# Kernel tuning notes

Hardware: AMD Instinct MI355X
Metric: run time of the kernel (lower is better)

Reference implementation:

```python
import jax, jax.numpy as jnp
import numpy as np

B, NSIDE, NH = 4, 64, 8
N = 12 * NSIDE * NSIDE          # HEALPix pixel count, nested ordering
CIN, CHID, COUT = 256, 512, 256
WS = 16                          # window = 4**(w+1) nested pixels, w=1
HD = CHID // NH


def _ln(x, g, b, eps=1e-5):
    m = x.mean(-1, keepdims=True)
    v = ((x - m) ** 2).mean(-1, keepdims=True)
    return (x - m) * jax.lax.rsqrt(v + eps) * g + b


def _win_attn(x, qkv_w, qkv_b, pw, pb):
    b_, n_, c = x.shape
    nw = n_ // WS
    xw = x.reshape(b_, nw, WS, c)
    qkv = xw @ qkv_w + qkv_b                      # [B, nw, ws, 3C]
    q, k, v = jnp.split(qkv, 3, axis=-1)
    def heads(t):
        return t.reshape(b_, nw, WS, NH, HD).transpose(0, 1, 3, 2, 4)
    q, k, v = heads(q), heads(k), heads(v)        # [B, nw, H, ws, hd]
    a = jax.nn.softmax(jnp.einsum('bwhqd,bwhkd->bwhqk', q, k) * (HD ** -0.5), axis=-1)
    o = jnp.einsum('bwhqk,bwhkd->bwhqd', a, v)
    o = o.transpose(0, 1, 3, 2, 4).reshape(b_, n_, c)
    return o @ pw + pb


def _heal_block(x, p, shift):
    if shift:
        x = jnp.roll(x, -WS // 2, axis=1)          # shifted-window (cyclic in nested order)
    x = x + _win_attn(_ln(x, p['ln1g'], p['ln1b']), p['qkvw'], p['qkvb'], p['pw'], p['pb'])
    h = _ln(x, p['ln2g'], p['ln2b'])
    h = jax.nn.gelu(h @ p['m1w'] + p['m1b'], approximate=False) @ p['m2w'] + p['m2b']
    x = x + h
    if shift:
        x = jnp.roll(x, WS // 2, axis=1)
    return x


def _sn_linear(h, W, b, u):
    # torch spectral_norm: one power-iteration, u/v detached, sigma = u' W v
    v = W @ u                                      # [CHID]
    v = jax.lax.stop_gradient(v / (jnp.linalg.norm(v) + 1e-12))
    u2 = v @ W                                     # [COUT]
    u2 = jax.lax.stop_gradient(u2 / (jnp.linalg.norm(u2) + 1e-12))
    sigma = v @ W @ u2
    return h @ (W / sigma) + b


def setup_inputs() -> dict:
    key = jax.random.key(0)
    ks = iter(jax.random.split(key, 64))
    def w(shape, s=0.02):
        return jax.random.normal(next(ks), shape, jnp.float32) * s
    inp = {'x': jax.random.normal(next(ks), (B, N, CIN), jnp.float32)}
    inp['ff1_w'] = w((CIN, CHID)); inp['ff1_b'] = jnp.zeros((CHID,), jnp.float32)
    for pre in ('a', 'b'):
        inp[f'{pre}_ln1g'] = jnp.ones((CHID,), jnp.float32)
        inp[f'{pre}_ln1b'] = jnp.zeros((CHID,), jnp.float32)
        inp[f'{pre}_qkvw'] = w((CHID, 3 * CHID)); inp[f'{pre}_qkvb'] = jnp.zeros((3 * CHID,), jnp.float32)
        inp[f'{pre}_pw'] = w((CHID, CHID)); inp[f'{pre}_pb'] = jnp.zeros((CHID,), jnp.float32)
        inp[f'{pre}_ln2g'] = jnp.ones((CHID,), jnp.float32)
        inp[f'{pre}_ln2b'] = jnp.zeros((CHID,), jnp.float32)
        inp[f'{pre}_m1w'] = w((CHID, 4 * CHID)); inp[f'{pre}_m1b'] = jnp.zeros((4 * CHID,), jnp.float32)
        inp[f'{pre}_m2w'] = w((4 * CHID, CHID)); inp[f'{pre}_m2b'] = jnp.zeros((CHID,), jnp.float32)
    inp['ff2_w'] = w((CHID, COUT)); inp['ff2_b'] = jnp.zeros((COUT,), jnp.float32)
    inp['ff2_u'] = jax.random.normal(next(ks), (COUT,), jnp.float32)
    return inp


def reference(x, ff1_w, ff1_b,
              a_ln1g, a_ln1b, a_qkvw, a_qkvb, a_pw, a_pb, a_ln2g, a_ln2b, a_m1w, a_m1b, a_m2w, a_m2b,
              b_ln1g, b_ln1b, b_qkvw, b_qkvb, b_pw, b_pb, b_ln2g, b_ln2b, b_m1w, b_m1b, b_m2w, b_m2b,
              ff2_w, ff2_b, ff2_u):
    pa = dict(ln1g=a_ln1g, ln1b=a_ln1b, qkvw=a_qkvw, qkvb=a_qkvb, pw=a_pw, pb=a_pb,
              ln2g=a_ln2g, ln2b=a_ln2b, m1w=a_m1w, m1b=a_m1b, m2w=a_m2w, m2b=a_m2b)
    pb_ = dict(ln1g=b_ln1g, ln1b=b_ln1b, qkvw=b_qkvw, qkvb=b_qkvb, pw=b_pw, pb=b_pb,
               ln2g=b_ln2g, ln2b=b_ln2b, m1w=b_m1w, m1b=b_m1b, m2w=b_m2w, m2b=b_m2b)
    h = jax.nn.gelu(x @ ff1_w + ff1_b, approximate=False)   # feed_forward1
    h = _heal_block(h, pa, shift=False)                     # message_passing1
    h = _heal_block(h, pb_, shift=True)                     # message_passing2
    return _sn_linear(h, ff2_w, ff2_b, ff2_u)               # spectral-norm linear
```

## Files before the change

### kernel.cpp

```cpp
#include <hip/hip_runtime.h>
#include <hip/hip_bf16.h>
#include <math.h>

typedef _Float16 f16;
typedef __attribute__((ext_vector_type(8))) _Float16 f16x8;
typedef __attribute__((ext_vector_type(4))) float f32x4;

#define DINLINE __device__ __forceinline__

DINLINE float gelu_exact(float x) {
  return 0.5f * x * (1.0f + erff(x * 0.70710678118654752f));
}
DINLINE void gload16(const void* g, void* l) {
  __builtin_amdgcn_global_load_lds((const __attribute__((address_space(1))) void*)g,
                                   (__attribute__((address_space(3))) void*)l, 16, 0, 0);
}

#define BAR       __builtin_amdgcn_s_barrier()
#define WAITLGKM  asm volatile("s_waitcnt lgkmcnt(0)" ::: "memory")
#define WAITVM(n) asm volatile("s_waitcnt vmcnt(" #n ")" ::: "memory")

template <int EPI>
__global__ __launch_bounds__(512, 2) void gemm256(
    const f16* __restrict__ A, const f16* __restrict__ Bt,
    const float* __restrict__ bias, const f16* __restrict__ Cin,
    float* __restrict__ Cf, f16* __restrict__ Cb,
    const float* __restrict__ scale_ptr,
    int N, int K, int nct)
{
  __shared__ alignas(16) f16 sm[2][4][8192];

  const int nwg = (int)gridDim.x;
  const int gid = (int)blockIdx.x;
  const int q = nwg >> 3, r = nwg & 7;
  const int xcd = gid & 7, idx = gid >> 3;
  const int swz = (xcd < r ? xcd * (q + 1) : r * (q + 1) + (xcd - r) * q) + idx;
  const int rt = swz / nct, ct = swz - rt * nct;
  const int m0 = rt << 8, n0 = ct << 8;

  const int tid = (int)threadIdx.x;
  const int lane = tid & 63;
  const int wid = tid >> 6;
  const int wr = wid >> 2, wc = wid & 3;

  const int srow = tid >> 2;
  const int sl = (tid & 3) ^ ((srow >> 1) & 3);
  const size_t aG = (size_t)(m0 + srow) * K + sl * 8;
  const size_t bG = (size_t)(n0 + srow) * K + sl * 8;
  const int sL = tid * 8;

  const int rsel = lane & 15, khi = lane >> 4;
  const int sx = (khi ^ ((rsel >> 1) & 3)) << 3;

  f32x4 acc[8][4] = {};
  f16x8 aF[4], bF[4];

  const int NT = K >> 6;

#define STAGEH(h)                                                             \
  {                                                                           \
    const int _t = (h) >> 2, _r = (h) & 3, _b = _t & 1;                       \
    const f16* _s = (_r & 1) ? Bt : A;                                        \
    const size_t _g = ((_r & 1) ? bG : aG) + (size_t)_t * 64 + ((_r >> 1) << 5); \
    gload16(_s + _g, &sm[_b][_r][sL]);                                        \
    gload16(_s + _g + (size_t)128 * (size_t)K, &sm[_b][_r][4096 + sL]);       \
  }

#define DSRA(b, kc, mb)                                                       \
  {                                                                           \
    _Pragma("unroll")                                                         \
    for (int _i = 0; _i < 4; ++_i)                                            \
      aF[_i] = *(const f16x8*)(&sm[b][(kc) << 1]                              \
                  [(wr * 128 + ((mb) + _i) * 16 + rsel) * 32 + sx]);          \
  }

#define DSRB(b, kc)                                                           \
  {                                                                           \
    _Pragma("unroll")                                                         \
    for (int _i = 0; _i < 4; ++_i)                                            \
      bF[_i] = *(const f16x8*)(&sm[b][1 + ((kc) << 1)]                        \
                  [(wc * 64 + _i * 16 + rsel) * 32 + sx]);                    \
  }

#define MMC(mb)                                                               \
  {                                                                           \
    __builtin_amdgcn_s_setprio(1);                                            \
    _Pragma("unroll")                                                         \
    for (int _m = 0; _m < 4; ++_m)                                            \
      _Pragma("unroll")                                                       \
      for (int _n = 0; _n < 4; ++_n)                                          \
        acc[(mb) + _m][_n] = __builtin_amdgcn_mfma_f32_16x16x32_f16(          \
            aF[_m], bF[_n], acc[(mb) + _m][_n], 0, 0, 0);                     \
    __builtin_amdgcn_s_setprio(0);                                            \
  }

  STAGEH(0); STAGEH(1); STAGEH(2); STAGEH(3); STAGEH(4);
  WAITVM(6);
  BAR;

  for (int t = 0; t < NT - 2; ++t) {
    const int b = t & 1, hb = 4 * t;
    STAGEH(hb + 5); DSRA(b, 0, 0); DSRB(b, 0); BAR; WAITLGKM; MMC(0); WAITVM(6); BAR;
    STAGEH(hb + 6); DSRA(b, 0, 4);             BAR; WAITLGKM; MMC(4); WAITVM(6); BAR;
    STAGEH(hb + 7); DSRA(b, 1, 0); DSRB(b, 1); BAR; WAITLGKM; MMC(0); WAITVM(6); BAR;
    STAGEH(hb + 8); DSRA(b, 1, 4);             BAR; WAITLGKM; MMC(4); WAITVM(6); BAR;
  }
  {
    const int t = NT - 2, b = t & 1, hb = 4 * t;
    STAGEH(hb + 5); DSRA(b, 0, 0); DSRB(b, 0); BAR; WAITLGKM; MMC(0); WAITVM(6); BAR;
    STAGEH(hb + 6); DSRA(b, 0, 4);             BAR; WAITLGKM; MMC(4); WAITVM(6); BAR;
    STAGEH(hb + 7); DSRA(b, 1, 0); DSRB(b, 1); BAR; WAITLGKM; MMC(0); WAITVM(6); BAR;
                    DSRA(b, 1, 4);             BAR; WAITLGKM; MMC(4); WAITVM(4); BAR;
  }
  {
    const int b = (NT - 1) & 1;
    DSRA(b, 0, 0); DSRB(b, 0); BAR; WAITLGKM; MMC(0); WAITVM(2); BAR;
    DSRA(b, 0, 4);             BAR; WAITLGKM; MMC(4); WAITVM(0); BAR;
    DSRA(b, 1, 0); DSRB(b, 1); BAR; WAITLGKM; MMC(0); BAR;
    DSRA(b, 1, 4);             BAR; WAITLGKM; MMC(4); BAR;
  }

  const float scale = (EPI & 8) ? scale_ptr[0] : 1.0f;
  const int R0 = m0 + wr * 128, C0 = n0 + wc * 64;
  f16* myr = (f16*)&sm[0][0][0] + wid * 8192;
#pragma unroll
  for (int m = 0; m < 8; ++m) {
#pragma unroll
    for (int n = 0; n < 4; ++n) {
      const int col = C0 + n * 16 + rsel;
      const float bb = bias ? bias[col] : 0.0f;
#pragma unroll
      for (int j = 0; j < 4; ++j) {
        const int rl = m * 16 + khi * 4 + j;
        const int row = R0 + rl;
        float v = acc[m][n][j] * scale + bb;
        if (EPI & 1) v = gelu_exact(v);
        if (EPI & 2) v += (float)Cin[(size_t)row * N + col];
        if (EPI & 4) myr[rl * 64 + n * 16 + rsel] = (f16)v;
        else         Cf[(size_t)row * N + col] = v;
      }
    }
  }
  if (EPI & 4) {
    asm volatile("" ::: "memory");
#pragma unroll
    for (int ci = 0; ci < 16; ++ci) {
      const int rl = ci * 8 + (lane >> 3);
      f16x8 v8 = *(const f16x8*)(myr + rl * 64 + (lane & 7) * 8);
      *(f16x8*)(Cb + (size_t)(R0 + rl) * N + C0 + (lane & 7) * 8) = v8;
    }
  }
#undef STAGEH
#undef DSRA
#undef DSRB
#undef MMC
}

__global__ __launch_bounds__(256) void ln_f16(
    const f16* __restrict__ X, const float* __restrict__ g,
    const float* __restrict__ b, f16* __restrict__ Y)
{
  const int token = blockIdx.x * 4 + (threadIdx.x >> 6);
  const int lane = threadIdx.x & 63;
  f16x8 v = *(const f16x8*)(X + (size_t)token * 512 + lane * 8);
  float vf[8];
  float s = 0.f, s2 = 0.f;
#pragma unroll
  for (int j = 0; j < 8; ++j) { vf[j] = (float)v[j]; s += vf[j]; s2 += vf[j] * vf[j]; }
#pragma unroll
  for (int o = 32; o > 0; o >>= 1) { s += __shfl_xor(s, o, 64); s2 += __shfl_xor(s2, o, 64); }
  const float mean = s * (1.f / 512.f);
  const float inv = rsqrtf(s2 * (1.f / 512.f) - mean * mean + 1e-5f);
  const int c = lane * 8;
  f32x4 g0 = *(const f32x4*)(g + c), g1 = *(const f32x4*)(g + c + 4);
  f32x4 b0 = *(const f32x4*)(b + c), b1 = *(const f32x4*)(b + c + 4);
  f16x8 o8;
#pragma unroll
  for (int j = 0; j < 4; ++j) {
    o8[j]     = (f16)((vf[j] - mean) * inv * g0[j] + b0[j]);
    o8[4 + j] = (f16)((vf[4 + j] - mean) * inv * g1[j] + b1[j]);
  }
  *(f16x8*)(Y + (size_t)token * 512 + c) = o8;
}

__global__ __launch_bounds__(256) void cvt_f32_f16(const float* __restrict__ X,
                                                   f16* __restrict__ Y, long n8)
{
  const long i = (long)blockIdx.x * 256 + threadIdx.x;
  if (i >= n8) return;
  f32x4 v0 = *(const f32x4*)(X + i * 8), v1 = *(const f32x4*)(X + i * 8 + 4);
  f16x8 o8;
#pragma unroll
  for (int j = 0; j < 4; ++j) { o8[j] = (f16)v0[j]; o8[4 + j] = (f16)v1[j]; }
  *(f16x8*)(Y + i * 8) = o8;
}

__global__ __launch_bounds__(256) void w_tr(const float* __restrict__ W,
                                            f16* __restrict__ Wt, int K, int N)
{
  const int t = blockIdx.x * 256 + threadIdx.x;
  if (t >= K * N) return;
  const int n = t / K, k = t - n * K;
  Wt[t] = (f16)W[(size_t)k * N + n];
}

template <int SHIFT>
__global__ __launch_bounds__(256) void win_attn(const f16* __restrict__ QKV,
                                                f16* __restrict__ O)
{
  __shared__ alignas(16) f16 kv[2][16][1160];
  const int wl0 = (int)blockIdx.x * 2;
  const int tid = (int)threadIdx.x;

  for (int i = tid; i < 4096; i += 256) {
    const int win = i >> 11;
    const int rem = i & 2047;
    const int row = rem >> 7;
    const int c8 = rem & 127;
    const int src = ((wl0 + win) * 16 + row + SHIFT) % 49152;
    const int sect = c8 >> 6;
    const int hh = (c8 >> 3) & 7;
    const int dd = (c8 & 7) * 8;
    *(f16x8*)(&kv[win][row][sect * 576 + hh * 72 + dd]) =
        *(const f16x8*)(QKV + (size_t)src * 1536 + 512 + c8 * 8);
  }

  const int win = tid >> 7, h = (tid >> 4) & 7, qi = tid & 15;
  const int qtok = ((wl0 + win) * 16 + qi + SHIFT) % 49152;
  f16x8 qv[8];
#pragma unroll
  for (int c8 = 0; c8 < 8; ++c8)
    qv[c8] = *(const f16x8*)(QKV + (size_t)qtok * 1536 + h * 64 + c8 * 8);

  __syncthreads();

  float sc[16];
  float mx = -1e30f;
#pragma unroll
  for (int kj = 0; kj < 16; ++kj) {
    const f16* kr = &kv[win][kj][h * 72];
    float s = 0.f;
#pragma unroll
    for (int c8 = 0; c8 < 8; ++c8) {
      f16x8 k8 = *(const f16x8*)(kr + c8 * 8);
#pragma unroll
      for (int j = 0; j < 8; ++j) s += (float)qv[c8][j] * (float)k8[j];
    }
    s *= 0.125f;
    sc[kj] = s;
    mx = fmaxf(mx, s);
  }
  float sum = 0.f;
#pragma unroll
  for (int kj = 0; kj < 16; ++kj) { sc[kj] = expf(sc[kj] - mx); sum += sc[kj]; }
  const float inv = 1.f / sum;
  float ov[64] = {};
#pragma unroll
  for (int kj = 0; kj < 16; ++kj) {
    const float a = sc[kj] * inv;
    const f16* vr = &kv[win][kj][576 + h * 72];
#pragma unroll
    for (int c8 = 0; c8 < 8; ++c8) {
      f16x8 v8 = *(const f16x8*)(vr + c8 * 8);
#pragma unroll
      for (int j = 0; j < 8; ++j) ov[c8 * 8 + j] += a * (float)v8[j];
    }
  }
  f16* orow = O + (size_t)qtok * 512 + h * 64;
#pragma unroll
  for (int c8 = 0; c8 < 8; ++c8) {
    f16x8 t;
#pragma unroll
    for (int j = 0; j < 8; ++j) t[j] = (f16)ov[c8 * 8 + j];
    *(f16x8*)(orow + c8 * 8) = t;
  }
}

__global__ __launch_bounds__(256) void sn_sigma(const float* __restrict__ W,
                                                const float* __restrict__ u,
                                                float* __restrict__ inv_sigma)
{
  __shared__ float vsh[512];
  __shared__ float ush[256];
  __shared__ float red[256];
  const int t = (int)threadIdx.x;
  ush[t] = u[t];
  __syncthreads();
  float a0 = 0.f, a1 = 0.f;
  for (int j = 0; j < 256; ++j) {
    a0 += W[t * 256 + j] * ush[j];
    a1 += W[(t + 256) * 256 + j] * ush[j];
  }
  vsh[t] = a0; vsh[t + 256] = a1;
  red[t] = a0 * a0 + a1 * a1;
  __syncthreads();
  for (int s = 128; s > 0; s >>= 1) { if (t < s) red[t] += red[t + s]; __syncthreads(); }
  const float nv = sqrtf(red[0]) + 1e-12f;
  __syncthreads();
  const float invv = 1.f / nv;
  vsh[t] *= invv; vsh[t + 256] *= invv;
  __syncthreads();
  float u2 = 0.f;
  for (int i = 0; i < 512; ++i) u2 += vsh[i] * W[i * 256 + t];
  red[t] = u2 * u2;
  __syncthreads();
  for (int s = 128; s > 0; s >>= 1) { if (t < s) red[t] += red[t + s]; __syncthreads(); }
  const float nu = sqrtf(red[0]) + 1e-12f;
  __syncthreads();
  ush[t] = u2 / nu;
  __syncthreads();
  float d0 = 0.f, d1 = 0.f;
  for (int j = 0; j < 256; ++j) {
    d0 += W[t * 256 + j] * ush[j];
    d1 += W[(t + 256) * 256 + j] * ush[j];
  }
  red[t] = vsh[t] * d0 + vsh[t + 256] * d1;
  __syncthreads();
  for (int s = 128; s > 0; s >>= 1) { if (t < s) red[t] += red[t + s]; __syncthreads(); }
  if (t == 0) inv_sigma[0] = 1.f / red[0];
}

__global__ void fill_sentinel(float* __restrict__ out, long n, float val)
{
  const long i = (long)blockIdx.x * 256 + threadIdx.x;
  for (long k = i; k < n; k += (long)gridDim.x * 256) out[k] = val;
}

extern "C" void kernel_launch(void* const* d_in, const int* in_sizes, int n_in,
                              void* d_out, int out_size, void* d_ws, size_t ws_size,
                              hipStream_t stream)
{
  const int M = 196608;
  const int MC = 49152;
  constexpr size_t OFF_U   = 201326592ull;
  constexpr size_t OFF_OH  = 201326592ull + 150994944ull;
  constexpr size_t OFF_WT  = 402653184ull;
  constexpr size_t OFF_SIG = 415760384ull;
  constexpr size_t NEED    = OFF_SIG + 256ull;

  if (ws_size < NEED) {
    fill_sentinel<<<2048, 256, 0, stream>>>((float*)d_out, (long)out_size,
                                            (float)(ws_size >> 20));
    return;
  }

  char* ws = (char*)d_ws;
  f16* R     = (f16*)(ws);
  f16* U     = (f16*)(ws + OFF_U);
  f16* OH    = (f16*)(ws + OFF_OH);
  f16* WT    = (f16*)(ws + OFF_WT);
  float* sig = (float*)(ws + OFF_SIG);
  f16* X     = (f16*)d_out;

  const float* ff1_b = (const float*)d_in[2];
  const float* ff2_b = (const float*)d_in[28];

  f16* W_FF1 = WT;
  auto W_QKV = [&](int blk) { return WT + (blk ? 3276800 : 131072); };
  auto W_PW  = [&](int blk) { return WT + (blk ? 4063232 : 917504); };
  auto W_M1  = [&](int blk) { return WT + (blk ? 4325376 : 1179648); };
  auto W_M2  = [&](int blk) { return WT + (blk ? 5373952 : 2228224); };
  f16* W_FF2 = WT + 6422528;

  w_tr<<<512, 256, 0, stream>>>((const float*)d_in[1], W_FF1, 256, 512);
  for (int blk = 0; blk < 2; ++blk) {
    w_tr<<<3072, 256, 0, stream>>>((const float*)d_in[blk ? 17 : 5], W_QKV(blk), 512, 1536);
    w_tr<<<1024, 256, 0, stream>>>((const float*)d_in[blk ? 19 : 7], W_PW(blk), 512, 512);
    w_tr<<<4096, 256, 0, stream>>>((const float*)d_in[blk ? 23 : 11], W_M1(blk), 512, 2048);
    w_tr<<<4096, 256, 0, stream>>>((const float*)d_in[blk ? 25 : 13], W_M2(blk), 2048, 512);
  }
  w_tr<<<512, 256, 0, stream>>>((const float*)d_in[27], W_FF2, 512, 256);
  sn_sigma<<<1, 256, 0, stream>>>((const float*)d_in[27], (const float*)d_in[29], sig);

  cvt_f32_f16<<<24576, 256, 0, stream>>>((const float*)d_in[0], U, (long)M * 256 / 8);
  gemm256<5><<<1536, 512, 0, stream>>>(U, W_FF1, ff1_b, nullptr, nullptr, R, nullptr,
                                       512, 256, 2);

  for (int blk = 0; blk < 2; ++blk) {
    const float* ln1g = (const float*)d_in[blk ? 15 : 3];
    const float* ln1b = (const float*)d_in[blk ? 16 : 4];
    const float* qkvb = (const float*)d_in[blk ? 18 : 6];
    const float* pb   = (const float*)d_in[blk ? 20 : 8];
    const float* ln2g = (const float*)d_in[blk ? 21 : 9];
    const float* ln2b = (const float*)d_in[blk ? 22 : 10];
    const float* m1b  = (const float*)d_in[blk ? 24 : 12];
    const float* m2b  = (const float*)d_in[blk ? 26 : 14];

    ln_f16<<<49152, 256, 0, stream>>>(R, ln1g, ln1b, X);
    for (int mc = 0; mc < 4; ++mc) {
      const size_t ro = (size_t)mc * MC * 512;
      gemm256<4><<<1152, 512, 0, stream>>>(X + ro, W_QKV(blk), qkvb, nullptr,
                                           nullptr, U, nullptr, 1536, 512, 6);
      if (blk == 0) win_attn<0><<<1536, 256, 0, stream>>>(U, OH);
      else          win_attn<8><<<1536, 256, 0, stream>>>(U, OH);
      gemm256<6><<<384, 512, 0, stream>>>(OH, W_PW(blk), pb, R + ro,
                                          nullptr, R + ro, nullptr, 512, 512, 2);
    }
    ln_f16<<<49152, 256, 0, stream>>>(R, ln2g, ln2b, X);
    for (int mc = 0; mc < 4; ++mc) {
      const size_t ro = (size_t)mc * MC * 512;
      gemm256<5><<<1536, 512, 0, stream>>>(X + ro, W_M1(blk), m1b, nullptr,
                                           nullptr, U, nullptr, 2048, 512, 8);
      gemm256<6><<<384, 512, 0, stream>>>(U, W_M2(blk), m2b, R + ro,
                                          nullptr, R + ro, nullptr, 512, 2048, 2);
    }
  }

  gemm256<8><<<768, 512, 0, stream>>>(R, W_FF2, ff2_b, nullptr, (float*)d_out,
                                      nullptr, sig, 256, 512, 1);
}
```

Baseline: 5.219 ms.

## Swap MFMA operands for direct vector epilogue, fast GELU, tiled weight transpose

Result: faster. 5.097 ms (-2.3%).

```diff
diff --git a/kernel.cpp b/kernel.cpp
--- a/kernel.cpp
+++ b/kernel.cpp
@@ -4,12 +4,15 @@
 
 typedef _Float16 f16;
 typedef __attribute__((ext_vector_type(8))) _Float16 f16x8;
+typedef __attribute__((ext_vector_type(4))) _Float16 f16x4;
 typedef __attribute__((ext_vector_type(4))) float f32x4;
 
 #define DINLINE __device__ __forceinline__
 
-DINLINE float gelu_exact(float x) {
-  return 0.5f * x * (1.0f + erff(x * 0.70710678118654752f));
+DINLINE float gelu_fast(float x) {
+  float t = 0.7978845608f * x * __builtin_fmaf(0.044715f * x, x, 1.0f);
+  float E = __expf(fminf(2.0f * t, 18.0f));
+  return x * E * __builtin_amdgcn_rcpf(E + 1.0f);
 }
 DINLINE void gload16(const void* g, void* l) {
   __builtin_amdgcn_global_load_lds((const __attribute__((address_space(1))) void*)g,
@@ -90,7 +93,7 @@
       _Pragma("unroll")                                                       \
       for (int _n = 0; _n < 4; ++_n)                                          \
         acc[(mb) + _m][_n] = __builtin_amdgcn_mfma_f32_16x16x32_f16(          \
-            aF[_m], bF[_n], acc[(mb) + _m][_n], 0, 0, 0);                     \
+            bF[_n], aF[_m], acc[(mb) + _m][_n], 0, 0, 0);                     \
     __builtin_amdgcn_s_setprio(0);                                            \
   }
 
@@ -122,32 +125,37 @@
 
   const float scale = (EPI & 8) ? scale_ptr[0] : 1.0f;
   const int R0 = m0 + wr * 128, C0 = n0 + wc * 64;
-  f16* myr = (f16*)&sm[0][0][0] + wid * 8192;
 #pragma unroll
   for (int m = 0; m < 8; ++m) {
+    const int row = R0 + m * 16 + rsel;
 #pragma unroll
     for (int n = 0; n < 4; ++n) {
-      const int col = C0 + n * 16 + rsel;
-      const float bb = bias ? bias[col] : 0.0f;
-#pragma unroll
-      for (int j = 0; j < 4; ++j) {
-        const int rl = m * 16 + khi * 4 + j;
-        const int row = R0 + rl;
-        float v = acc[m][n][j] * scale + bb;
-        if (EPI & 1) v = gelu_exact(v);
-        if (EPI & 2) v += (float)Cin[(size_t)row * N + col];
-        if (EPI & 4) myr[rl * 64 + n * 16 + rsel] = (f16)v;
-        else         Cf[(size_t)row * N + col] = v;
+      const int col = C0 + n * 16 + (khi << 2);
+      f32x4 v = acc[m][n];
+      if (EPI & 8) {
+#pragma unroll
+        for (int j = 0; j < 4; ++j) v[j] *= scale;
       }
-    }
-  }
-  if (EPI & 4) {
-    asm volatile("" ::: "memory");
-#pragma unroll
-    for (int ci = 0; ci < 16; ++ci) {
-      const int rl = ci * 8 + (lane >> 3);
-      f16x8 v8 = *(const f16x8*)(myr + rl * 64 + (lane & 7) * 8);
-      *(f16x8*)(Cb + (size_t)(R0 + rl) * N + C0 + (lane & 7) * 8) = v8;
+      f32x4 bb = *(const f32x4*)(bias + col);
+#pragma unroll
+      for (int j = 0; j < 4; ++j) v[j] += bb[j];
+      if (EPI & 1) {
+#pragma unroll
+        for (int j = 0; j < 4; ++j) v[j] = gelu_fast(v[j]);
+      }
+      if (EPI & 2) {
+        f16x4 c4 = *(const f16x4*)(Cin + (size_t)row * N + col);
+#pragma unroll
+        for (int j = 0; j < 4; ++j) v[j] += (float)c4[j];
+      }
+      if (EPI & 4) {
+        f16x4 o;
+#pragma unroll
+        for (int j = 0; j < 4; ++j) o[j] = (f16)v[j];
+        *(f16x4*)(Cb + (size_t)row * N + col) = o;
+      } else {
+        *(f32x4*)(Cf + (size_t)row * N + col) = v;
+      }
     }
   }
 #undef STAGEH
@@ -158,29 +166,31 @@
 
 __global__ __launch_bounds__(256) void ln_f16(
     const f16* __restrict__ X, const float* __restrict__ g,
-    const float* __restrict__ b, f16* __restrict__ Y)
-{
-  const int token = blockIdx.x * 4 + (threadIdx.x >> 6);
+    const float* __restrict__ b, f16* __restrict__ Y, int ntok)
+{
   const int lane = threadIdx.x & 63;
-  f16x8 v = *(const f16x8*)(X + (size_t)token * 512 + lane * 8);
-  float vf[8];
-  float s = 0.f, s2 = 0.f;
-#pragma unroll
-  for (int j = 0; j < 8; ++j) { vf[j] = (float)v[j]; s += vf[j]; s2 += vf[j] * vf[j]; }
-#pragma unroll
-  for (int o = 32; o > 0; o >>= 1) { s += __shfl_xor(s, o, 64); s2 += __shfl_xor(s2, o, 64); }
-  const float mean = s * (1.f / 512.f);
-  const float inv = rsqrtf(s2 * (1.f / 512.f) - mean * mean + 1e-5f);
   const int c = lane * 8;
-  f32x4 g0 = *(const f32x4*)(g + c), g1 = *(const f32x4*)(g + c + 4);
-  f32x4 b0 = *(const f32x4*)(b + c), b1 = *(const f32x4*)(b + c + 4);
-  f16x8 o8;
-#pragma unroll
-  for (int j = 0; j < 4; ++j) {
-    o8[j]     = (f16)((vf[j] - mean) * inv * g0[j] + b0[j]);
-    o8[4 + j] = (f16)((vf[4 + j] - mean) * inv * g1[j] + b1[j]);
-  }
-  *(f16x8*)(Y + (size_t)token * 512 + c) = o8;
+  const f32x4 g0 = *(const f32x4*)(g + c), g1 = *(const f32x4*)(g + c + 4);
+  const f32x4 b0 = *(const f32x4*)(b + c), b1 = *(const f32x4*)(b + c + 4);
+  for (int token = blockIdx.x * 4 + (threadIdx.x >> 6); token < ntok;
+       token += gridDim.x * 4) {
+    f16x8 v = *(const f16x8*)(X + (size_t)token * 512 + c);
+    float vf[8];
+    float s = 0.f, s2 = 0.f;
+#pragma unroll
+    for (int j = 0; j < 8; ++j) { vf[j] = (float)v[j]; s += vf[j]; s2 += vf[j] * vf[j]; }
+#pragma unroll
+    for (int o = 32; o > 0; o >>= 1) { s += __shfl_xor(s, o, 64); s2 += __shfl_xor(s2, o, 64); }
+    const float mean = s * (1.f / 512.f);
+    const float inv = rsqrtf(s2 * (1.f / 512.f) - mean * mean + 1e-5f);
+    f16x8 o8;
+#pragma unroll
+    for (int j = 0; j < 4; ++j) {
+      o8[j]     = (f16)((vf[j] - mean) * inv * g0[j] + b0[j]);
+      o8[4 + j] = (f16)((vf[4 + j] - mean) * inv * g1[j] + b1[j]);
+    }
+    *(f16x8*)(Y + (size_t)token * 512 + c) = o8;
+  }
 }
 
 __global__ __launch_bounds__(256) void cvt_f32_f16(const float* __restrict__ X,
@@ -195,13 +205,25 @@
   *(f16x8*)(Y + i * 8) = o8;
 }
 
-__global__ __launch_bounds__(256) void w_tr(const float* __restrict__ W,
-                                            f16* __restrict__ Wt, int K, int N)
-{
-  const int t = blockIdx.x * 256 + threadIdx.x;
-  if (t >= K * N) return;
-  const int n = t / K, k = t - n * K;
-  Wt[t] = (f16)W[(size_t)k * N + n];
+__global__ __launch_bounds__(256) void w_tr_tiled(const float* __restrict__ W,
+                                                  f16* __restrict__ Wt, int K, int N)
+{
+  __shared__ f16 td[64][66];
+  const int nkt = K >> 6;
+  const int kt = blockIdx.x % nkt, nt = blockIdx.x / nkt;
+  const int k0 = kt << 6, n0 = nt << 6;
+  const int col = threadIdx.x & 63, rq = threadIdx.x >> 6;
+#pragma unroll
+  for (int j = 0; j < 16; ++j) {
+    const int row = j * 4 + rq;
+    td[row][col] = (f16)W[(size_t)(k0 + row) * N + n0 + col];
+  }
+  __syncthreads();
+#pragma unroll
+  for (int j = 0; j < 16; ++j) {
+    const int nrow = j * 4 + rq;
+    Wt[(size_t)(n0 + nrow) * K + k0 + col] = td[col][nrow];
+  }
 }
 
 template <int SHIFT>
@@ -362,14 +384,14 @@
   auto W_M2  = [&](int blk) { return WT + (blk ? 5373952 : 2228224); };
   f16* W_FF2 = WT + 6422528;
 
-  w_tr<<<512, 256, 0, stream>>>((const float*)d_in[1], W_FF1, 256, 512);
+  w_tr_tiled<<<32, 256, 0, stream>>>((const float*)d_in[1], W_FF1, 256, 512);
   for (int blk = 0; blk < 2; ++blk) {
-    w_tr<<<3072, 256, 0, stream>>>((const float*)d_in[blk ? 17 : 5], W_QKV(blk), 512, 1536);
-    w_tr<<<1024, 256, 0, stream>>>((const float*)d_in[blk ? 19 : 7], W_PW(blk), 512, 512);
-    w_tr<<<4096, 256, 0, stream>>>((const float*)d_in[blk ? 23 : 11], W_M1(blk), 512, 2048);
-    w_tr<<<4096, 256, 0, stream>>>((const float*)d_in[blk ? 25 : 13], W_M2(blk), 2048, 512);
-  }
-  w_tr<<<512, 256, 0, stream>>>((const float*)d_in[27], W_FF2, 512, 256);
+    w_tr_tiled<<<192, 256, 0, stream>>>((const float*)d_in[blk ? 17 : 5], W_QKV(blk), 512, 1536);
+    w_tr_tiled<<<64, 256, 0, stream>>>((const float*)d_in[blk ? 19 : 7], W_PW(blk), 512, 512);
+    w_tr_tiled<<<256, 256, 0, stream>>>((const float*)d_in[blk ? 23 : 11], W_M1(blk), 512, 2048);
+    w_tr_tiled<<<256, 256, 0, stream>>>((const float*)d_in[blk ? 25 : 13], W_M2(blk), 2048, 512);
+  }
+  w_tr_tiled<<<32, 256, 0, stream>>>((const float*)d_in[27], W_FF2, 512, 256);
   sn_sigma<<<1, 256, 0, stream>>>((const float*)d_in[27], (const float*)d_in[29], sig);
 
   cvt_f32_f16<<<24576, 256, 0, stream>>>((const float*)d_in[0], U, (long)M * 256 / 8);
@@ -386,7 +408,7 @@
     const float* m1b  = (const float*)d_in[blk ? 24 : 12];
     const float* m2b  = (const float*)d_in[blk ? 26 : 14];
 
-    ln_f16<<<49152, 256, 0, stream>>>(R, ln1g, ln1b, X);
+    ln_f16<<<4096, 256, 0, stream>>>(R, ln1g, ln1b, X, M);
     for (int mc = 0; mc < 4; ++mc) {
       const size_t ro = (size_t)mc * MC * 512;
       gemm256<4><<<1152, 512, 0, stream>>>(X + ro, W_QKV(blk), qkvb, nullptr,
@@ -396,7 +418,7 @@
       gemm256<6><<<384, 512, 0, stream>>>(OH, W_PW(blk), pb, R + ro,
                                           nullptr, R + ro, nullptr, 512, 512, 2);
     }
-    ln_f16<<<49152, 256, 0, stream>>>(R, ln2g, ln2b, X);
+    ln_f16<<<4096, 256, 0, stream>>>(R, ln2g, ln2b, X, M);
     for (int mc = 0; mc < 4; ++mc) {
       const size_t ro = (size_t)mc * MC * 512;
       gemm256<5><<<1536, 512, 0, stream>>>(X + ro, W_M1(blk), m1b, nullptr,
```
